# Optimization experiments

Hardware: AMD Instinct MI355X
Metric: run time of the kernel (lower is better)

Reference implementation:

```python
import jax, jax.numpy as jnp
import numpy as np

NUM_EXPERTS = 4


def _conv1x1(w, b, x):
    # w: [out,in], b: [out], x: [B,in,H,W]
    return jnp.einsum('oc,bchw->bohw', w, x) + b[None, :, None, None]


def _sobel(x):
    c = x.shape[1]
    kx = jnp.array([[-1., 0., 1.], [-2., 0., 2.], [-1., 0., 1.]], dtype=x.dtype)
    ky = jnp.array([[-1., -2., -1.], [0., 0., 0.], [1., 2., 1.]], dtype=x.dtype)
    wx = jnp.broadcast_to(kx[None, None], (c, 1, 3, 3))
    wy = jnp.broadcast_to(ky[None, None], (c, 1, 3, 3))
    dn = ('NCHW', 'OIHW', 'NCHW')
    gx = jax.lax.conv_general_dilated(x, wx, (1, 1), [(1, 1), (1, 1)],
                                      dimension_numbers=dn, feature_group_count=c)
    gy = jax.lax.conv_general_dilated(x, wy, (1, 1), [(1, 1), (1, 1)],
                                      dimension_numbers=dn, feature_group_count=c)
    return gx, gy


def _bilinear_sample(x, gx, gy):
    # torch F.grid_sample(mode='bilinear', padding_mode='zeros', align_corners=False)
    # x: [B,C,H,W]; gx, gy: [B,Hs,Ws] normalized coords in [-1,1]
    B, C, H, W = x.shape
    ix = ((gx + 1.0) * W - 1.0) * 0.5
    iy = ((gy + 1.0) * H - 1.0) * 0.5
    x0 = jnp.floor(ix)
    y0 = jnp.floor(iy)
    wx1 = ix - x0
    wx0 = 1.0 - wx1
    wy1 = iy - y0
    wy0 = 1.0 - wy1
    xf = x.reshape(B, C, H * W)

    def gather(xc, yc):
        valid = (xc >= 0) & (xc <= W - 1) & (yc >= 0) & (yc <= H - 1)
        xi = jnp.clip(xc, 0, W - 1).astype(jnp.int32)
        yi = jnp.clip(yc, 0, H - 1).astype(jnp.int32)
        idx = yi * W + xi  # [B,Hs,Ws]
        v = jax.vmap(lambda xb, ib: xb[:, ib])(xf, idx)  # [B,C,Hs,Ws]
        return v * valid[:, None].astype(x.dtype)

    return (gather(x0, y0) * (wx0 * wy0)[:, None]
            + gather(x0 + 1, y0) * (wx1 * wy0)[:, None]
            + gather(x0, y0 + 1) * (wx0 * wy1)[:, None]
            + gather(x0 + 1, y0 + 1) * (wx1 * wy1)[:, None])


def _forward(x, wc_e, we_e, wb1, bb1, wb2, bb2, wr, br, wo, bo, wcv, bcv, scale, scale2):
    B, c, h, w = x.shape
    sh = round(h * scale)
    sw = round(w * scale2)

    grad_x, grad_y = _sobel(x)

    # relative-offset coordinate embedding, [1,4,sh,sw]
    ih = (jnp.arange(sh, dtype=x.dtype) + 0.5) / scale
    coor_h = ih - jnp.floor(ih + 0.001) - 0.5  # [sh]
    iw = (jnp.arange(sw, dtype=x.dtype) + 0.5) / scale2
    coor_w = iw - jnp.floor(iw + 0.001) - 0.5  # [sw]
    inp = jnp.stack([
        jnp.full((sh, sw), 1.0 / scale2, dtype=x.dtype),
        jnp.full((sh, sw), 1.0 / scale, dtype=x.dtype),
        jnp.broadcast_to(coor_h[:, None], (sh, sw)),
        jnp.broadcast_to(coor_w[None, :], (sh, sw)),
    ], axis=0)[None]

    emb = jax.nn.relu(_conv1x1(wb2, bb2, jax.nn.relu(_conv1x1(wb1, bb1, inp))))
    offset = _conv1x1(wo, bo, emb)                 # [1,2,sh,sw]
    routing = jax.nn.sigmoid(_conv1x1(wr, br, emb))  # [1,E,sh,sw]

    # per-pixel soft mixture of expert compress/expand matrices
    rw = routing.reshape(NUM_EXPERTS, sh * sw).T   # [N,E]
    wc = (rw @ wc_e.reshape(NUM_EXPERTS, -1)).reshape(sh, sw, c // 8, c)
    we = (rw @ we_e.reshape(NUM_EXPERTS, -1)).reshape(sh, sw, c, c // 8)

    feat = _conv1x1(wcv, bcv, jnp.concatenate([x, grad_x, grad_y], axis=1))  # [B,64,h,w]

    # base grid (align_corners=True-style normalization, as in the source) + learned offsets
    gx0 = ((jnp.arange(sw, dtype=x.dtype) + 0.5) / scale2 - 0.5) * 2.0 / (w - 1) - 1.0
    gy0 = ((jnp.arange(sh, dtype=x.dtype) + 0.5) / scale - 0.5) * 2.0 / (h - 1) - 1.0
    gx = jnp.broadcast_to(gx0[None, None, :] + offset[:, 0] * (2.0 / (w - 1)), (B, sh, sw))
    gy = jnp.broadcast_to(gy0[None, :, None] + offset[:, 1] * (2.0 / (h - 1)), (B, sh, sw))

    fea0 = _bilinear_sample(feat, gx, gy)          # [B,64,sh,sw]

    mid = jnp.einsum('hwkc,bchw->bhwk', wc, fea0)  # per-pixel compress (k=C//8)
    out = jnp.einsum('hwck,bhwk->bchw', we, mid)   # per-pixel expand
    return out + fea0


def setup_inputs() -> dict:
    key = jax.random.key(0)
    ks = jax.random.split(key, 13)
    s = 0.05
    return {
        'x': jax.random.normal(ks[0], (2, 64, 192, 192), jnp.float32),
        'weight_compress': jax.random.normal(ks[1], (4, 8, 64), jnp.float32) * s,
        'weight_expand': jax.random.normal(ks[2], (4, 64, 8), jnp.float32) * s,
        'w_body1': jax.random.normal(ks[3], (64, 4), jnp.float32) * s,
        'b_body1': jax.random.normal(ks[4], (64,), jnp.float32) * s,
        'w_body2': jax.random.normal(ks[5], (64, 64), jnp.float32) * s,
        'b_body2': jax.random.normal(ks[6], (64,), jnp.float32) * s,
        'w_routing': jax.random.normal(ks[7], (4, 64), jnp.float32) * s,
        'b_routing': jax.random.normal(ks[8], (4,), jnp.float32) * s,
        'w_offset': jax.random.normal(ks[9], (2, 64), jnp.float32) * s,
        'b_offset': jax.random.normal(ks[10], (2,), jnp.float32) * s,
        'w_conv': jax.random.normal(ks[11], (64, 192), jnp.float32) * s,
        'b_conv': jax.random.normal(ks[12], (64,), jnp.float32) * s,
        'scale': 2,
        'scale2': 2,
    }


def reference(x, weight_compress, weight_expand, w_body1, b_body1, w_body2, b_body2,
              w_routing, b_routing, w_offset, b_offset, w_conv, b_conv, scale, scale2):
    return _forward(x, weight_compress, weight_expand, w_body1, b_body1, w_body2, b_body2,
                    w_routing, b_routing, w_offset, b_offset, w_conv, b_conv, scale, scale2)
```

## Files before the change

### kernel.cpp

```cpp
#include <hip/hip_runtime.h>
#include <hip/hip_bf16.h>
#include <math.h>

#define BN  2
#define CN  64
#define HN  192
#define WN  192
#define SH  384
#define SW  384
#define HW  (HN * WN)
#define NPIX (BN * HN * WN)

typedef __attribute__((ext_vector_type(8))) short bf16x8;
typedef __attribute__((ext_vector_type(4))) float f32x4;

#define ROWS  2
#define CPAD  72
#define MAINB (BN * (HN / ROWS) * 3)
#define TBLB  64

__device__ inline unsigned short f2bf(float f) {
    unsigned int u = __float_as_uint(f);
    u += 0x7fffu + ((u >> 16) & 1u);
    return (unsigned short)(u >> 16);
}
__device__ inline unsigned int pkbf(float a, float b) {
    return (unsigned int)f2bf(a) | ((unsigned int)f2bf(b) << 16);
}

__device__ inline void run_mlp(int lane, float in0, float in1, float chv, float cwv,
    const float* __restrict__ wb1, const float* __restrict__ bb1,
    const float* __restrict__ wb2, const float* __restrict__ bb2,
    const float* __restrict__ wr,  const float* __restrict__ wo, float p[6])
{
    float4 w1 = ((const float4*)wb1)[lane];
    float h1 = fmaxf(bb1[lane] + w1.x * in0 + w1.y * in1 + w1.z * chv + w1.w * cwv, 0.f);
    const float4* w2row = (const float4*)(wb2 + lane * 64);
    float acc = bb2[lane];
#pragma unroll
    for (int q = 0; q < 16; ++q) {
        float4 wv = w2row[q];
        acc += wv.x * __shfl(h1, q * 4 + 0)
             + wv.y * __shfl(h1, q * 4 + 1)
             + wv.z * __shfl(h1, q * 4 + 2)
             + wv.w * __shfl(h1, q * 4 + 3);
    }
    float h2 = fmaxf(acc, 0.f);
#pragma unroll
    for (int e = 0; e < 4; ++e) p[e] = wr[e * 64 + lane] * h2;
#pragma unroll
    for (int e = 0; e < 2; ++e) p[4 + e] = wo[e * 64 + lane] * h2;
#pragma unroll
    for (int m = 1; m < 64; m <<= 1) {
#pragma unroll
        for (int e = 0; e < 6; ++e) p[e] += __shfl_xor(p[e], m);
    }
}

__global__ __launch_bounds__(256) void feat_table_kernel(
    const float* __restrict__ x,
    const float* __restrict__ wcv,
    const float* __restrict__ bcv,
    float* __restrict__ feat,
    const float* __restrict__ wb1, const float* __restrict__ bb1,
    const float* __restrict__ wb2, const float* __restrict__ bb2,
    const float* __restrict__ wr,  const float* __restrict__ br,
    const float* __restrict__ wo,  const float* __restrict__ bo,
    const float* __restrict__ wce, const float* __restrict__ wee,
    const int* __restrict__ scale_p, const int* __restrict__ scale2_p,
    float* __restrict__ tblEntry, unsigned short* __restrict__ tblM)
{
    __shared__ __attribute__((aligned(16))) unsigned short smem_u16[4 * 66 * CPAD];

    int tid  = threadIdx.x;
    int lane = tid & 63;

    if (blockIdx.x >= MAINB) {
        float* wcmL = (float*)smem_u16;
        float* wemL = wcmL + 1024;
        float* reL  = wemL + 1024;

        int sc = scale_p[0], sc2 = scale2_p[0];
        float scale = (float)sc, scale2 = (float)sc2;
        float in0 = 1.f / scale2, in1 = 1.f / scale;
        bool fast = (sc2 == 2 && sc <= 16);
        int tb = blockIdx.x - MAINB;

        if (fast) {
            int pi = tb;
            if (pi >= sc) return;
            if (tid < 64) {
                float ih = (pi + 0.5f) / scale;
                float chv = ih - floorf(ih + 0.001f) - 0.5f;
                float p0[6], p1[6];
                {
                    float iw = 0.5f / scale2;
                    float cwv = iw - floorf(iw + 0.001f) - 0.5f;
                    run_mlp(lane, in0, in1, chv, cwv, wb1, bb1, wb2, bb2, wr, wo, p0);
                }
                {
                    float iw = 1.5f / scale2;
                    float cwv = iw - floorf(iw + 0.001f) - 0.5f;
                    run_mlp(lane, in0, in1, chv, cwv, wb1, bb1, wb2, bb2, wr, wo, p1);
                }
                if (lane == 0) {
                    float* t0 = tblEntry + (pi * 2 + 0) * 8;
                    float* t1 = tblEntry + (pi * 2 + 1) * 8;
#pragma unroll
                    for (int e = 0; e < 4; ++e) {
                        float rE = 1.f / (1.f + expf(-(p0[e] + br[e])));
                        float rO = 1.f / (1.f + expf(-(p1[e] + br[e])));
                        t0[e] = rE; t1[e] = rO;
                        reL[e] = rE; reL[4 + e] = rO;
                    }
                    t0[4] = p0[4] + bo[0]; t0[5] = p0[5] + bo[1];
                    t1[4] = p1[4] + bo[0]; t1[5] = p1[5] + bo[1];
                }
            }
            __syncthreads();
            float reE0 = reL[0], reE1 = reL[1], reE2 = reL[2], reE3 = reL[3];
            float reO0 = reL[4], reO1 = reL[5], reO2 = reL[6], reO3 = reL[7];
            for (int idx = tid; idx < 512; idx += 256) {
                float a = wce[idx], bq = wce[512 + idx], c = wce[1024 + idx], d = wce[1536 + idx];
                wcmL[idx]       = reE0 * a + reE1 * bq + reE2 * c + reE3 * d;
                wcmL[512 + idx] = reO0 * a + reO1 * bq + reO2 * c + reO3 * d;
                float e_ = wee[idx], f = wee[512 + idx], g = wee[1024 + idx], h = wee[1536 + idx];
                wemL[idx]       = reE0 * e_ + reE1 * f + reE2 * g + reE3 * h;
                wemL[512 + idx] = reO0 * e_ + reO1 * f + reO2 * g + reO3 * h;
            }
            __syncthreads();
            int co  = tid >> 2;
            int ci0 = (tid & 3) << 4;
            float w0[8], w1[8];
#pragma unroll
            for (int k = 0; k < 8; ++k) {
                w0[k] = wemL[co * 8 + k];
                w1[k] = wemL[512 + co * 8 + k];
            }
            unsigned short* tbp = tblM + (size_t)pi * 2 * 4096;
#pragma unroll
            for (int cc = 0; cc < 16; ++cc) {
                int ci = ci0 + cc;
                float m0 = 0.f, m1 = 0.f;
#pragma unroll
                for (int k = 0; k < 8; ++k) {
                    m0 += w0[k] * wcmL[k * 64 + ci];
                    m1 += w1[k] * wcmL[512 + k * 64 + ci];
                }
                tbp[co * 64 + ci]        = f2bf(0.5f * (m0 + m1));
                tbp[4096 + co * 64 + ci] = f2bf(0.5f * (m0 - m1));
            }
        } else {
            int w_ = (tb * 256 + tid) >> 6;
            if (w_ >= sc * sc2) return;
            int pi = w_ / sc2, pj = w_ - pi * sc2;
            float ih = (pi + 0.5f) / scale;
            float chv = ih - floorf(ih + 0.001f) - 0.5f;
            float iw = (pj + 0.5f) / scale2;
            float cwv = iw - floorf(iw + 0.001f) - 0.5f;
            float p[6];
            run_mlp(lane, in0, in1, chv, cwv, wb1, bb1, wb2, bb2, wr, wo, p);
            if (lane == 0) {
                float* tp = tblEntry + w_ * 8;
#pragma unroll
                for (int e = 0; e < 4; ++e) tp[e] = 1.f / (1.f + expf(-(p[e] + br[e])));
                tp[4] = p[4] + bo[0];
                tp[5] = p[5] + bo[1];
            }
        }
        return;
    }

    int bi = blockIdx.x;
    int jt = bi % 3;
    int t2 = bi / 3;
    int it = t2 % (HN / ROWS);
    int b  = t2 / (HN / ROWS);
    int i0 = it * ROWS;
    int j0 = jt * 64;
    int w  = __builtin_amdgcn_readfirstlane(tid >> 6);

    int row = lane & 15;
    int q   = lane >> 4;

    const float KXc[9] = {-1.f, 0.f, 1.f, -2.f, 0.f, 2.f, -1.f, 0.f, 1.f};
    const float KYc[9] = {-1.f, -2.f, -1.f, 0.f, 0.f, 0.f, 1.f, 2.f, 1.f};
    bf16x8 afrag[9][2];
    {
        int o = (w << 4) + row;
        const float* wp = wcv + o * 192;
        float v0[2][8], v1[2][8], v2[2][8];
#pragma unroll
        for (int kc = 0; kc < 2; ++kc) {
            int kb = kc * 32 + q * 8;
            float4 a0 = *(const float4*)(wp + kb);
            float4 a1 = *(const float4*)(wp + kb + 4);
            float4 b0 = *(const float4*)(wp + 64 + kb);
            float4 b1 = *(const float4*)(wp + 64 + kb + 4);
            float4 c0 = *(const float4*)(wp + 128 + kb);
            float4 c1 = *(const float4*)(wp + 128 + kb + 4);
            v0[kc][0]=a0.x; v0[kc][1]=a0.y; v0[kc][2]=a0.z; v0[kc][3]=a0.w;
            v0[kc][4]=a1.x; v0[kc][5]=a1.y; v0[kc][6]=a1.z; v0[kc][7]=a1.w;
            v1[kc][0]=b0.x; v1[kc][1]=b0.y; v1[kc][2]=b0.z; v1[kc][3]=b0.w;
            v1[kc][4]=b1.x; v1[kc][5]=b1.y; v1[kc][6]=b1.z; v1[kc][7]=b1.w;
            v2[kc][0]=c0.x; v2[kc][1]=c0.y; v2[kc][2]=c0.z; v2[kc][3]=c0.w;
            v2[kc][4]=c1.x; v2[kc][5]=c1.y; v2[kc][6]=c1.z; v2[kc][7]=c1.w;
        }
#pragma unroll
        for (int t = 0; t < 9; ++t) {
#pragma unroll
            for (int kc = 0; kc < 2; ++kc) {
                bf16x8 a;
#pragma unroll
                for (int e = 0; e < 8; ++e) {
                    float f = v1[kc][e] * KXc[t] + v2[kc][e] * KYc[t];
                    if (t == 4) f += v0[kc][e];
                    a[e] = (short)f2bf(f);
                }
                afrag[t][kc] = a;
            }
        }
    }

    {
        int sr = i0 - 1 + w;
        bool rok = (sr >= 0) && (sr < HN);
        int src = rok ? sr : 0;
        int hc = j0 - 1 + lane;
        bool cok = (hc >= 0) && (hc < WN);
        int hcc = cok ? hc : 0;
        float msk = (rok && cok) ? 1.f : 0.f;
        const float* p = x + (size_t)b * CN * HW + (size_t)src * WN + hcc;
        unsigned short* xrow = smem_u16 + (w * 66 + lane) * CPAD;
#pragma unroll 4
        for (int k = 0; k < 16; ++k) {
            int c0 = k << 2;
            float a0 = p[0] * msk;
            float a1 = p[(size_t)HW] * msk;
            float a2 = p[2 * (size_t)HW] * msk;
            float a3 = p[3 * (size_t)HW] * msk;
            uint2 uu;
            uu.x = pkbf(a0, a1);
            uu.y = pkbf(a2, a3);
            *(uint2*)(xrow + c0) = uu;
            p += 4 * (size_t)HW;
        }
        if (lane < 32) {
            int colx = 64 + (lane & 1);
            int c0 = (lane >> 1) << 2;
            int hx = j0 - 1 + colx;
            bool cokx = (hx < WN);
            int hxc = cokx ? hx : 0;
            float mskx = (rok && cokx) ? 1.f : 0.f;
            const float* px = x + ((size_t)b * CN + c0) * HW + (size_t)src * WN + hxc;
            float a0 = px[0] * mskx;
            float a1 = px[(size_t)HW] * mskx;
            float a2 = px[2 * (size_t)HW] * mskx;
            float a3 = px[3 * (size_t)HW] * mskx;
            uint2 uu;
            uu.x = pkbf(a0, a1);
            uu.y = pkbf(a2, a3);
            *(uint2*)(smem_u16 + (w * 66 + colx) * CPAD + c0) = uu;
        }
    }

    __syncthreads();

    f32x4 acc[2][4] = {};
    const unsigned short* bb0 = smem_u16 + row * CPAD + (q << 3);
#pragma unroll
    for (int ro = 0; ro < 2; ++ro) {
#pragma unroll
        for (int nt = 0; nt < 4; ++nt) {
#pragma unroll
            for (int t = 0; t < 9; ++t) {
                int a_ = t / 3, dxi = t - a_ * 3;
#pragma unroll
                for (int kc = 0; kc < 2; ++kc) {
                    bf16x8 bv = *(const bf16x8*)(bb0 + ((ro + a_) * 66 + nt * 16 + dxi) * CPAD + kc * 32);
                    acc[ro][nt] = __builtin_amdgcn_mfma_f32_16x16x32_bf16(afrag[t][kc], bv, acc[ro][nt], 0, 0, 0);
                }
            }
        }
    }

#pragma unroll
    for (int ro = 0; ro < 2; ++ro) {
        size_t rb0 = (size_t)b * CN * HW + (size_t)(i0 + ro) * WN + j0 + row;
#pragma unroll
        for (int rr = 0; rr < 4; ++rr) {
            int oc = (w << 4) + q * 4 + rr;
            float bias = bcv[oc];
            size_t rowb = rb0 + (size_t)oc * HW;
#pragma unroll
            for (int nt = 0; nt < 4; ++nt)
                feat[rowb + nt * 16] = acc[ro][nt][rr] + bias;
        }
    }
}

#define BKP 72
__global__ __launch_bounds__(256) void out_kernel(
    const float* __restrict__ feat,
    const float* __restrict__ tblEntry,
    const unsigned short* __restrict__ tblM,
    const float* __restrict__ wce,
    const float* __restrict__ wee,
    const int* __restrict__ scale_p, const int* __restrict__ scale2_p,
    float* __restrict__ out)
{
    __shared__ __attribute__((aligned(16))) float smem[64 * 65 + 64 * (BKP / 2)];
    float* fea32 = smem;
    unsigned short* Bsv = (unsigned short*)(smem + 64 * 65);
    float* midp = smem;

    int Bk = blockIdx.x;
    int T = gridDim.x;
    int t = ((T & 7) == 0) ? ((Bk & 7) * (T >> 3) + (Bk >> 3)) : Bk;

    int tid = threadIdx.x;
    int g = __builtin_amdgcn_readfirstlane(tid >> 6);
    int lane = tid & 63;
    int pix0 = t * 64;
    int b = pix0 / (SH * SW);
    int r0 = pix0 - b * SH * SW;
    int i = r0 / SW;
    int j0 = r0 - i * SW;
    int j = j0 + lane;
    int r = r0 + lane;

    int sc = scale_p[0], sc2 = scale2_p[0];
    float scale = (float)sc, scale2 = (float)sc2;
    int pi = i - (i / sc) * sc;
    int pj = j - (j / sc2) * sc2;
    int entry = pi * sc2 + pj;
    float offx = tblEntry[entry * 8 + 4];
    float offy = tblEntry[entry * 8 + 5];

    const float inv_wm1 = 2.f / (float)(WN - 1);
    const float inv_hm1 = 2.f / (float)(HN - 1);
    float gx = ((j + 0.5f) / scale2 - 0.5f) * inv_wm1 - 1.f + offx * inv_wm1;
    float gy = ((i + 0.5f) / scale  - 0.5f) * inv_hm1 - 1.f + offy * inv_hm1;

    float ix = ((gx + 1.f) * WN - 1.f) * 0.5f;
    float iy = ((gy + 1.f) * HN - 1.f) * 0.5f;
    float fx0 = floorf(ix), fy0 = floorf(iy);
    int x0 = (int)fx0, y0 = (int)fy0;
    float wx1 = ix - fx0, wx0 = 1.f - wx1;
    float wy1 = iy - fy0, wy0 = 1.f - wy1;

    bool vx0 = (x0 >= 0) && (x0 <= WN - 1);
    bool vx1 = (x0 + 1 >= 0) && (x0 + 1 <= WN - 1);
    bool vy0 = (y0 >= 0) && (y0 <= HN - 1);
    bool vy1 = (y0 + 1 >= 0) && (y0 + 1 <= HN - 1);
    bool v00 = vx0 && vy0, v10 = vx1 && vy0, v01 = vx0 && vy1, v11 = vx1 && vy1;
    float w00 = wx0 * wy0, w10 = wx1 * wy0, w01 = wx0 * wy1, w11 = wx1 * wy1;

    int i00 = y0 * WN + x0;
    int i10 = i00 + 1;
    int i01 = i00 + WN;
    int i11 = i01 + 1;

    const float* fb = feat + (size_t)b * CN * HW;

    float f0[16];
#pragma unroll
    for (int cc = 0; cc < 16; ++cc) {
        const float* fc = fb + (size_t)(g * 16 + cc) * HW;
        float a  = v00 ? fc[i00] : 0.f;
        float bq = v10 ? fc[i10] : 0.f;
        float cq = v01 ? fc[i01] : 0.f;
        float dq = v11 ? fc[i11] : 0.f;
        f0[cc] = a * w00 + bq * w10 + cq * w01 + dq * w11;
    }

    bool fast = (sc2 == 2 && sc <= 16);
    if (fast) {
        int px = lane;
#pragma unroll
        for (int cc = 0; cc < 16; ++cc)
            fea32[px * 65 + g * 16 + cc] = f0[cc];
#pragma unroll
        for (int cc = 0; cc < 16; cc += 2) {
            unsigned int pk = (unsigned int)f2bf(f0[cc]) | ((unsigned int)f2bf(f0[cc + 1]) << 16);
            *(unsigned int*)(Bsv + px * BKP + g * 16 + cc) = pk;
        }

        int row = lane & 15;
        int kb  = (lane >> 4) << 3;
        const unsigned short* Mb = tblM + (size_t)pi * 2 * 4096 + (g * 16 + row) * 64 + kb;
        bf16x8 a1[2], a2[2];
        a1[0] = *(const bf16x8*)(Mb);
        a1[1] = *(const bf16x8*)(Mb + 32);
        a2[0] = *(const bf16x8*)(Mb + 4096);
        a2[1] = *(const bf16x8*)(Mb + 4096 + 32);

        __syncthreads();

        f32x4 acc1[4] = {}, acc2[4] = {};
        const unsigned short* bp = Bsv + (lane & 15) * BKP + kb;
#pragma unroll
        for (int nt = 0; nt < 4; ++nt) {
            const unsigned short* bnt = bp + nt * 16 * BKP;
#pragma unroll
            for (int ks = 0; ks < 2; ++ks) {
                bf16x8 bf = *(const bf16x8*)(bnt + ks * 32);
                acc1[nt] = __builtin_amdgcn_mfma_f32_16x16x32_bf16(a1[ks], bf, acc1[nt], 0, 0, 0);
                acc2[nt] = __builtin_amdgcn_mfma_f32_16x16x32_bf16(a2[ks], bf, acc2[nt], 0, 0, 0);
            }
        }

        int q = lane >> 4;
#pragma unroll
        for (int rr = 0; rr < 4; ++rr) {
            int c = g * 16 + q * 4 + rr;
            size_t rowb = (size_t)(b * CN + c) * SH * SW + r0;
#pragma unroll
            for (int nt = 0; nt < 4; ++nt) {
                int n = (lane & 15) + nt * 16;
                float sgn = (n & 1) ? -1.f : 1.f;
                float v = fea32[n * 65 + c] + acc1[nt][rr] + sgn * acc2[nt][rr];
                out[rowb + n] = v;
            }
        }
    } else {
        float4 rw = *(const float4*)(tblEntry + entry * 8);
        float re[4] = {rw.x, rw.y, rw.z, rw.w};
        float part[4][8];
#pragma unroll
        for (int e = 0; e < 4; ++e) {
#pragma unroll
            for (int k = 0; k < 8; ++k) {
                const float* wrow = wce + (e * 8 + k) * 64 + g * 16;
                float d = 0.f;
#pragma unroll
                for (int cc = 0; cc < 16; ++cc) d += wrow[cc] * f0[cc];
                part[e][k] = d;
            }
        }
#pragma unroll
        for (int k = 0; k < 8; ++k) {
            float m = re[0] * part[0][k] + re[1] * part[1][k]
                    + re[2] * part[2][k] + re[3] * part[3][k];
            midp[(g * 64 + lane) * 9 + k] = m;
        }
        __syncthreads();
        float mid[8];
#pragma unroll
        for (int k = 0; k < 8; ++k)
            mid[k] = midp[(0 * 64 + lane) * 9 + k] + midp[(1 * 64 + lane) * 9 + k]
                   + midp[(2 * 64 + lane) * 9 + k] + midp[(3 * 64 + lane) * 9 + k];
#pragma unroll
        for (int cc = 0; cc < 16; ++cc) {
            int c = g * 16 + cc;
            float v = f0[cc];
#pragma unroll
            for (int e = 0; e < 4; ++e) {
                const float* wrow = wee + (e * 64 + c) * 8;
                float d = 0.f;
#pragma unroll
                for (int k = 0; k < 8; ++k) d += wrow[k] * mid[k];
                v += re[e] * d;
            }
            out[(size_t)(b * CN + c) * SH * SW + r] = v;
        }
    }
}

extern "C" void kernel_launch(void* const* d_in, const int* in_sizes, int n_in,
                              void* d_out, int out_size, void* d_ws, size_t ws_size,
                              hipStream_t stream) {
    const float* x    = (const float*)d_in[0];
    const float* wce  = (const float*)d_in[1];
    const float* wee  = (const float*)d_in[2];
    const float* wb1  = (const float*)d_in[3];
    const float* bb1  = (const float*)d_in[4];
    const float* wb2  = (const float*)d_in[5];
    const float* bb2  = (const float*)d_in[6];
    const float* wr   = (const float*)d_in[7];
    const float* br   = (const float*)d_in[8];
    const float* wo   = (const float*)d_in[9];
    const float* bo   = (const float*)d_in[10];
    const float* wcv  = (const float*)d_in[11];
    const float* bcv  = (const float*)d_in[12];
    const int*   scale  = (const int*)d_in[13];
    const int*   scale2 = (const int*)d_in[14];
    float* out = (float*)d_out;

    float* feat     = (float*)d_ws;
    float* tblEntry = feat + (size_t)BN * CN * HW;
    unsigned short* tblM = (unsigned short*)(tblEntry + 256 * 8);

    feat_table_kernel<<<MAINB + TBLB, 256, 0, stream>>>(
        x, wcv, bcv, feat, wb1, bb1, wb2, bb2, wr, br, wo, bo,
        wce, wee, scale, scale2, tblEntry, tblM);
    out_kernel<<<BN * SH * SW / 64, 256, 0, stream>>>(feat, tblEntry, tblM,
                                                      wce, wee, scale, scale2, out);
}
```

Baseline: 150.6 us.

## Process one output row per block in fused sobel-conv tile kernel

Changes the feature conv tile from two output rows per block to one, doubling the number of main blocks and shrinking the shared halo buffer from 4 to 3 rows. The halo load is re-partitioned so 198 threads each load one column across all 64 channels, with 8 channels per 16-byte LDS store instead of 4. This aims for more parallelism and occupancy. In exchange it loses vertical halo reuse: 3 input rows are loaded per output row instead of 4 per 2, which raises global read traffic, and the per-block weight fragment setup is repeated twice as often.

```diff
diff --git a/kernel.cpp b/kernel.cpp
--- a/kernel.cpp
+++ b/kernel.cpp
@@ -14,9 +14,8 @@
 typedef __attribute__((ext_vector_type(8))) short bf16x8;
 typedef __attribute__((ext_vector_type(4))) float f32x4;
 
-#define ROWS  2
 #define CPAD  72
-#define MAINB (BN * (HN / ROWS) * 3)
+#define MAINB (BN * HN * 3)
 #define TBLB  64
 
 __device__ inline unsigned short f2bf(float f) {
@@ -70,7 +69,7 @@
     const int* __restrict__ scale_p, const int* __restrict__ scale2_p,
     float* __restrict__ tblEntry, unsigned short* __restrict__ tblM)
 {
-    __shared__ __attribute__((aligned(16))) unsigned short smem_u16[4 * 66 * CPAD];
+    __shared__ __attribute__((aligned(16))) unsigned short smem_u16[3 * 66 * CPAD];
 
     int tid  = threadIdx.x;
     int lane = tid & 63;
@@ -174,9 +173,8 @@
     int bi = blockIdx.x;
     int jt = bi % 3;
     int t2 = bi / 3;
-    int it = t2 % (HN / ROWS);
-    int b  = t2 / (HN / ROWS);
-    int i0 = it * ROWS;
+    int i0 = t2 % HN;
+    int b  = t2 / HN;
     int j0 = jt * 64;
     int w  = __builtin_amdgcn_readfirstlane(tid >> 6);
 
@@ -222,80 +220,64 @@
         }
     }
 
-    {
-        int sr = i0 - 1 + w;
+    if (tid < 3 * 66) {
+        int rowi = tid / 66;
+        int col  = tid - rowi * 66;
+        int sr = i0 - 1 + rowi;
         bool rok = (sr >= 0) && (sr < HN);
         int src = rok ? sr : 0;
-        int hc = j0 - 1 + lane;
+        int hc = j0 - 1 + col;
         bool cok = (hc >= 0) && (hc < WN);
         int hcc = cok ? hc : 0;
         float msk = (rok && cok) ? 1.f : 0.f;
         const float* p = x + (size_t)b * CN * HW + (size_t)src * WN + hcc;
-        unsigned short* xrow = smem_u16 + (w * 66 + lane) * CPAD;
+        unsigned short* xrow = smem_u16 + (rowi * 66 + col) * CPAD;
 #pragma unroll 4
-        for (int k = 0; k < 16; ++k) {
-            int c0 = k << 2;
-            float a0 = p[0] * msk;
-            float a1 = p[(size_t)HW] * msk;
+        for (int k = 0; k < 8; ++k) {
+            float a0 = p[0]              * msk;
+            float a1 = p[(size_t)HW]     * msk;
             float a2 = p[2 * (size_t)HW] * msk;
             float a3 = p[3 * (size_t)HW] * msk;
-            uint2 uu;
+            float a4 = p[4 * (size_t)HW] * msk;
+            float a5 = p[5 * (size_t)HW] * msk;
+            float a6 = p[6 * (size_t)HW] * msk;
+            float a7 = p[7 * (size_t)HW] * msk;
+            uint4 uu;
             uu.x = pkbf(a0, a1);
             uu.y = pkbf(a2, a3);
-            *(uint2*)(xrow + c0) = uu;
-            p += 4 * (size_t)HW;
-        }
-        if (lane < 32) {
-            int colx = 64 + (lane & 1);
-            int c0 = (lane >> 1) << 2;
-            int hx = j0 - 1 + colx;
-            bool cokx = (hx < WN);
-            int hxc = cokx ? hx : 0;
-            float mskx = (rok && cokx) ? 1.f : 0.f;
-            const float* px = x + ((size_t)b * CN + c0) * HW + (size_t)src * WN + hxc;
-            float a0 = px[0] * mskx;
-            float a1 = px[(size_t)HW] * mskx;
-            float a2 = px[2 * (size_t)HW] * mskx;
-            float a3 = px[3 * (size_t)HW] * mskx;
-            uint2 uu;
-            uu.x = pkbf(a0, a1);
-            uu.y = pkbf(a2, a3);
-            *(uint2*)(smem_u16 + (w * 66 + colx) * CPAD + c0) = uu;
+            uu.z = pkbf(a4, a5);
+            uu.w = pkbf(a6, a7);
+            *(uint4*)(xrow + (k << 3)) = uu;
+            p += 8 * (size_t)HW;
         }
     }
 
     __syncthreads();
 
-    f32x4 acc[2][4] = {};
+    f32x4 acc[4] = {};
     const unsigned short* bb0 = smem_u16 + row * CPAD + (q << 3);
 #pragma unroll
-    for (int ro = 0; ro < 2; ++ro) {
-#pragma unroll
-        for (int nt = 0; nt < 4; ++nt) {
-#pragma unroll
-            for (int t = 0; t < 9; ++t) {
-                int a_ = t / 3, dxi = t - a_ * 3;
-#pragma unroll
-                for (int kc = 0; kc < 2; ++kc) {
-                    bf16x8 bv = *(const bf16x8*)(bb0 + ((ro + a_) * 66 + nt * 16 + dxi) * CPAD + kc * 32);
-                    acc[ro][nt] = __builtin_amdgcn_mfma_f32_16x16x32_bf16(afrag[t][kc], bv, acc[ro][nt], 0, 0, 0);
-                }
-            }
-        }
-    }
-
-#pragma unroll
-    for (int ro = 0; ro < 2; ++ro) {
-        size_t rb0 = (size_t)b * CN * HW + (size_t)(i0 + ro) * WN + j0 + row;
-#pragma unroll
-        for (int rr = 0; rr < 4; ++rr) {
-            int oc = (w << 4) + q * 4 + rr;
-            float bias = bcv[oc];
-            size_t rowb = rb0 + (size_t)oc * HW;
-#pragma unroll
-            for (int nt = 0; nt < 4; ++nt)
-                feat[rowb + nt * 16] = acc[ro][nt][rr] + bias;
-        }
+    for (int nt = 0; nt < 4; ++nt) {
+#pragma unroll
+        for (int t = 0; t < 9; ++t) {
+            int a_ = t / 3, dxi = t - a_ * 3;
+#pragma unroll
+            for (int kc = 0; kc < 2; ++kc) {
+                bf16x8 bv = *(const bf16x8*)(bb0 + (a_ * 66 + nt * 16 + dxi) * CPAD + kc * 32);
+                acc[nt] = __builtin_amdgcn_mfma_f32_16x16x32_bf16(afrag[t][kc], bv, acc[nt], 0, 0, 0);
+            }
+        }
+    }
+
+    size_t rb0 = (size_t)b * CN * HW + (size_t)i0 * WN + j0 + row;
+#pragma unroll
+    for (int rr = 0; rr < 4; ++rr) {
+        int oc = (w << 4) + q * 4 + rr;
+        float bias = bcv[oc];
+        size_t rowb = rb0 + (size_t)oc * HW;
+#pragma unroll
+        for (int nt = 0; nt < 4; ++nt)
+            feat[rowb + nt * 16] = acc[nt][rr] + bias;
     }
 }
 
```

New measurement: 152.8 us. No clear change (+1.5%).
